# Kernel optimization log

Hardware: AMD Instinct MI355X
Metric: run time of the kernel (lower is better)

## Reference

```python
import jax, jax.numpy as jnp
import numpy as np

SEQ_LEN = 2048
EMB_DIM = 1024
HIDDEN = 1024
VOCAB = 50257
OUT = 50257


def setup_inputs() -> dict:
    key = jax.random.key(0)
    ks = jax.random.split(key, 8)
    s = 0.02
    input_seq = jax.random.randint(ks[0], (SEQ_LEN,), 0, VOCAB)
    emb = jax.random.normal(ks[1], (VOCAB, EMB_DIM), dtype=jnp.float32) * s
    # PyTorch nn.LSTM params: weight_ih [4H, E], weight_hh [4H, H], biases [4H]
    W_ih = jax.random.normal(ks[2], (4 * HIDDEN, EMB_DIM), dtype=jnp.float32) * s
    W_hh = jax.random.normal(ks[3], (4 * HIDDEN, HIDDEN), dtype=jnp.float32) * s
    b_ih = jax.random.normal(ks[4], (4 * HIDDEN,), dtype=jnp.float32) * s
    b_hh = jax.random.normal(ks[5], (4 * HIDDEN,), dtype=jnp.float32) * s
    W_out = jax.random.normal(ks[6], (OUT, HIDDEN), dtype=jnp.float32) * s
    b_out = jax.random.normal(ks[7], (OUT,), dtype=jnp.float32) * s
    return {"input_seq": input_seq, "emb": emb, "W_ih": W_ih, "W_hh": W_hh,
            "b_ih": b_ih, "b_hh": b_hh, "W_out": W_out, "b_out": b_out}


def _lstm_forward(x, W_ih, W_hh, b_ih, b_hh):
    # x: [S, E]; batch dim (=1 in the torch module) is collapsed away.
    H = W_hh.shape[1]
    # Precompute input contribution to all gates for every timestep: [S, 4H]
    x_gates = x @ W_ih.T + (b_ih + b_hh)

    def step(carry, xg):
        h, c = carry
        g = xg + h @ W_hh.T  # [4H]
        i, f, gg, o = jnp.split(g, 4)  # PyTorch gate order: i, f, g, o
        i = jax.nn.sigmoid(i)
        f = jax.nn.sigmoid(f)
        gg = jnp.tanh(gg)
        o = jax.nn.sigmoid(o)
        c = f * c + i * gg
        h = o * jnp.tanh(c)
        return (h, c), h

    h0 = jnp.zeros((H,), dtype=x.dtype)
    c0 = jnp.zeros((H,), dtype=x.dtype)
    _, hs = jax.lax.scan(step, (h0, c0), x_gates)
    return hs  # [S, H]


def reference(input_seq, emb, W_ih, W_hh, b_ih, b_hh, W_out, b_out):
    x = emb[input_seq]  # [S, E] embedding lookup
    hs = _lstm_forward(x, W_ih, W_hh, b_ih, b_hh)  # [S, H]
    logits = hs @ W_out.T + b_out  # [S, OUT]
    return jax.nn.log_softmax(logits, axis=1)
```

## Files before the change

kernel.cpp:

```cpp
#include <hip/hip_runtime.h>
#include <hip/hip_bf16.h>

#define SEQ 2048
#define EMB 1024
#define HID 1024
#define G4  4096
#define VOC 50257
#define VPAD 50304
#define KDIM 1024

typedef short bhalf8 __attribute__((ext_vector_type(8)));
typedef float f32x4  __attribute__((ext_vector_type(4)));

typedef __attribute__((address_space(3))) void lds_void;
typedef __attribute__((address_space(1))) const void gbl_cvoid;

__device__ __forceinline__ void direct_lds16(void* lds, const void* g) {
    __builtin_amdgcn_global_load_lds((gbl_cvoid*)g, (lds_void*)lds, 16, 0, 0);
}

__device__ __forceinline__ unsigned short f2b(float f) {
    unsigned u = __float_as_uint(f);
    unsigned r = u + 0x7fffu + ((u >> 16) & 1u);
    return (unsigned short)(r >> 16);
}

__global__ void f32_to_bf16_k(const float* __restrict__ src, unsigned short* __restrict__ dst,
                              long n_src, long n_dst) {
    long i = ((long)blockIdx.x * 256 + threadIdx.x) * 4;
    if (i >= n_dst) return;
    unsigned short o0 = 0, o1 = 0, o2 = 0, o3 = 0;
    if (i < n_src) {
        f32x4 v = *(const f32x4*)&src[i];
        o0 = f2b(v[0]); o1 = f2b(v[1]); o2 = f2b(v[2]); o3 = f2b(v[3]);
    }
    ushort4 o; o.x = o0; o.y = o1; o.z = o2; o.w = o3;
    *(ushort4*)&dst[i] = o;
}

__global__ void embed_cvt_k(const int* __restrict__ seq, const float* __restrict__ emb,
                            unsigned short* __restrict__ xb) {
    int s = blockIdx.x;
    int k = threadIdx.x * 4;
    long row = (long)seq[s] * EMB;
    f32x4 v = *(const f32x4*)&emb[row + k];
    ushort4 o; o.x = f2b(v[0]); o.y = f2b(v[1]); o.z = f2b(v[2]); o.w = f2b(v[3]);
    *(ushort4*)&xb[(long)s * EMB + k] = o;
}

__global__ void bias_sum_k(const float* __restrict__ a, const float* __restrict__ b,
                           float* __restrict__ o) {
    int i = blockIdx.x * 256 + threadIdx.x;
    if (i < G4) o[i] = a[i] + b[i];
}

__global__ __launch_bounds__(256)
void gemm_bt_k(const unsigned short* __restrict__ A, const unsigned short* __restrict__ Bt,
               const float* __restrict__ bias, float* __restrict__ C,
               int M, int Nreal, int K, int ldc) {
    __shared__ unsigned short lA[128 * 64];
    __shared__ unsigned short lB[128 * 64];
    const int tid  = threadIdx.x;
    const int wave = tid >> 6;
    const int lane = tid & 63;
    const int m0 = blockIdx.x * 128;
    const int n0 = blockIdx.y * 128;
    const int wm = (wave >> 1) * 64;
    const int wn = (wave & 1) * 64;
    const int quad = lane >> 4, l16 = lane & 15;
    const int srow = lane >> 3;
    const int scol = (lane & 7) * 8;

    f32x4 acc[4][4] = {};

    for (int k0 = 0; k0 < K; k0 += 64) {
#pragma unroll
        for (int c = 0; c < 4; ++c) {
            int r0 = wave * 32 + c * 8;
            const unsigned short* ga = A  + (long)(m0 + r0 + srow) * K + k0 + scol;
            direct_lds16(&lA[r0 * 64], ga);
            const unsigned short* gb = Bt + (long)(n0 + r0 + srow) * K + k0 + scol;
            direct_lds16(&lB[r0 * 64], gb);
        }
        __syncthreads();
#pragma unroll
        for (int kk = 0; kk < 2; ++kk) {
            bhalf8 af[4], bf[4];
#pragma unroll
            for (int i = 0; i < 4; ++i) {
                af[i] = *(const bhalf8*)&lA[(wm + i * 16 + l16) * 64 + kk * 32 + quad * 8];
                bf[i] = *(const bhalf8*)&lB[(wn + i * 16 + l16) * 64 + kk * 32 + quad * 8];
            }
#pragma unroll
            for (int i = 0; i < 4; ++i)
#pragma unroll
                for (int j = 0; j < 4; ++j)
                    acc[i][j] = __builtin_amdgcn_mfma_f32_16x16x32_bf16(af[i], bf[j], acc[i][j], 0, 0, 0);
        }
        __syncthreads();
    }
#pragma unroll
    for (int i = 0; i < 4; ++i) {
        int gm = m0 + wm + i * 16 + quad * 4;
#pragma unroll
        for (int j = 0; j < 4; ++j) {
            int gn = n0 + wn + j * 16 + l16;
            if (gn < Nreal) {
                float bv = bias[gn];
#pragma unroll
                for (int r = 0; r < 4; ++r)
                    C[(long)(gm + r) * ldc + gn] = acc[i][j][r] + bv;
            }
        }
    }
}

__global__ __launch_bounds__(256, 1)
void lstm_seq_k(const float* __restrict__ W_hh, const float* __restrict__ xg,
                unsigned short* __restrict__ hs_b, unsigned long long* __restrict__ hbuf) {
    const int tid = threadIdx.x;
    const int wg  = blockIdx.x;
    const int lr  = tid >> 4;
    const int seg = tid & 15;
    const int gate = lr >> 2;
    const int ul   = lr & 3;
    const int u    = wg * 4 + ul;
    const int grow = gate * HID + u;

    __shared__ float h_lds[HID];
    __shared__ float g_lds[4][4];

    f32x4 w[16];
#pragma unroll
    for (int m = 0; m < 16; ++m)
        w[m] = *(const f32x4*)&W_hh[(long)grow * HID + (m * 16 + seg) * 4];

#pragma unroll
    for (int q = 0; q < 4; ++q) h_lds[tid + q * 256] = 0.f;
    float c = 0.f;
    __syncthreads();

    for (int t = 0; t < SEQ; ++t) {
        float xgv = (seg == 0) ? xg[(long)t * G4 + grow] : 0.f;
        if (t > 0) {
            const unsigned long long want = (unsigned long long)t;
            unsigned long long* src = &hbuf[((t - 1) & 1) * HID];
#pragma unroll
            for (int q = 0; q < 4; ++q) {
                int e = tid + q * 256;
                unsigned long long v;
                do {
                    v = __hip_atomic_load(&src[e], __ATOMIC_RELAXED, __HIP_MEMORY_SCOPE_AGENT);
                } while ((v >> 32) != want);
                h_lds[e] = __uint_as_float((unsigned)v);
            }
        }
        __syncthreads();

        float acc = 0.f;
        const f32x4* h4 = (const f32x4*)h_lds;
#pragma unroll
        for (int m = 0; m < 16; ++m) {
            f32x4 hv = h4[m * 16 + seg];
            acc += w[m][0] * hv[0] + w[m][1] * hv[1] + w[m][2] * hv[2] + w[m][3] * hv[3];
        }
        acc += __shfl_xor(acc, 8);
        acc += __shfl_xor(acc, 4);
        acc += __shfl_xor(acc, 2);
        acc += __shfl_xor(acc, 1);

        if (seg == 0) {
            float g = acc + xgv;
            float a = (gate == 2) ? tanhf(g) : 1.f / (1.f + __expf(-g));
            g_lds[gate][ul] = a;
        }
        __syncthreads();
        if (tid < 4) {
            float iv = g_lds[0][tid], fv = g_lds[1][tid], gv = g_lds[2][tid], ov = g_lds[3][tid];
            c = fv * c + iv * gv;
            float h = ov * tanhf(c);
            int ug = wg * 4 + tid;
            hs_b[(long)t * HID + ug] = f2b(h);
            unsigned long long pk = ((unsigned long long)(t + 1) << 32) | (unsigned long long)__float_as_uint(h);
            __hip_atomic_store(&hbuf[(t & 1) * HID + ug], pk, __ATOMIC_RELAXED, __HIP_MEMORY_SCOPE_AGENT);
        }
        __syncthreads();
    }
}

__global__ __launch_bounds__(256)
void log_softmax_k(float* __restrict__ X) {
    const int tid = threadIdx.x;
    const long base = (long)blockIdx.x * VOC;
    float* p = X + base;
    const int head = (4 - (int)(base & 3)) & 3;
    const int n4 = (VOC - head) >> 2;
    const int tail_start = head + n4 * 4;
    f32x4* p4 = (f32x4*)(p + head);

    float m = -INFINITY, s = 0.f;
    auto upd = [&](float x) {
        float nm = fmaxf(m, x);
        s = s * __expf(m - nm) + __expf(x - nm);
        m = nm;
    };
    for (int i = tid; i < n4; i += 256) {
        f32x4 v = p4[i];
        upd(v[0]); upd(v[1]); upd(v[2]); upd(v[3]);
    }
    if (tid == 0) {
        for (int i = 0; i < head; ++i) upd(p[i]);
        for (int i = tail_start; i < VOC; ++i) upd(p[i]);
    }
#pragma unroll
    for (int o = 32; o; o >>= 1) {
        float m2 = __shfl_xor(m, o), s2 = __shfl_xor(s, o);
        float nm = fmaxf(m, m2);
        s = s * __expf(m - nm) + s2 * __expf(m2 - nm);
        m = nm;
    }
    __shared__ float sm[4], ss[4], sL;
    if ((tid & 63) == 0) { sm[tid >> 6] = m; ss[tid >> 6] = s; }
    __syncthreads();
    if (tid == 0) {
        m = sm[0]; s = ss[0];
        for (int wv = 1; wv < 4; ++wv) {
            float m2 = sm[wv], s2 = ss[wv];
            float nm = fmaxf(m, m2);
            s = s * __expf(m - nm) + s2 * __expf(m2 - nm);
            m = nm;
        }
        sL = m + __logf(s);
    }
    __syncthreads();
    const float L = sL;
    for (int i = tid; i < n4; i += 256) {
        f32x4 v = p4[i];
        v[0] -= L; v[1] -= L; v[2] -= L; v[3] -= L;
        p4[i] = v;
    }
    if (tid == 0) {
        for (int i = 0; i < head; ++i) p[i] -= L;
        for (int i = tail_start; i < VOC; ++i) p[i] -= L;
    }
}

extern "C" void kernel_launch(void* const* d_in, const int* in_sizes, int n_in,
                              void* d_out, int out_size, void* d_ws, size_t ws_size,
                              hipStream_t stream) {
    const int*   seq   = (const int*)d_in[0];
    const float* emb   = (const float*)d_in[1];
    const float* W_ih  = (const float*)d_in[2];
    const float* W_hh  = (const float*)d_in[3];
    const float* b_ih  = (const float*)d_in[4];
    const float* b_hh  = (const float*)d_in[5];
    const float* W_out = (const float*)d_in[6];
    const float* b_out = (const float*)d_in[7];
    float* out = (float*)d_out;

    size_t off = 0;
    auto carve = [&](size_t bytes) {
        void* p = (char*)d_ws + off;
        off += (bytes + 255) & ~(size_t)255;
        return p;
    };
    unsigned short* wWout = (unsigned short*)carve((size_t)VPAD * KDIM * 2);
    unsigned short* wWih  = (unsigned short*)carve((size_t)G4 * KDIM * 2);
    unsigned short* wX    = (unsigned short*)carve((size_t)SEQ * EMB * 2);
    unsigned short* wHs   = (unsigned short*)carve((size_t)SEQ * HID * 2);
    float*          wXg   = (float*)carve((size_t)SEQ * G4 * 4);
    float*          wBsum = (float*)carve((size_t)G4 * 4);
    unsigned long long* wHbuf = (unsigned long long*)carve((size_t)2 * HID * 8);

    f32_to_bf16_k<<<(int)(((size_t)VPAD * KDIM / 4 + 255) / 256), 256, 0, stream>>>(
        W_out, wWout, (long)VOC * KDIM, (long)VPAD * KDIM);
    f32_to_bf16_k<<<(int)(((size_t)G4 * KDIM / 4 + 255) / 256), 256, 0, stream>>>(
        W_ih, wWih, (long)G4 * KDIM, (long)G4 * KDIM);
    embed_cvt_k<<<SEQ, 256, 0, stream>>>(seq, emb, wX);
    bias_sum_k<<<(G4 + 255) / 256, 256, 0, stream>>>(b_ih, b_hh, wBsum);

    gemm_bt_k<<<dim3(SEQ / 128, G4 / 128), 256, 0, stream>>>(
        wX, wWih, wBsum, wXg, SEQ, G4, KDIM, G4);

    lstm_seq_k<<<256, 256, 0, stream>>>(W_hh, wXg, wHs, wHbuf);

    gemm_bt_k<<<dim3(SEQ / 128, VPAD / 128), 256, 0, stream>>>(
        wHs, wWout, b_out, out, SEQ, VOC, KDIM, VOC);

    log_softmax_k<<<SEQ, 256, 0, stream>>>(out);
}
```

Baseline: 6.589 ms.

## Restructure LSTM step to one wave per unit with shuffles and double-buffered LDS

Remaps threads so each wave owns one hidden unit's four gates, which lets gate values be exchanged with wave shuffles instead of LDS. Double-buffering the h vector in LDS removes two of the three per-step block barriers, and the hidden-state store now happens before the bf16 output write. The four global polling loads are issued together before any check, the dot product is split into four independent accumulators, and tanh is computed through a scaled sigmoid with fast exp. This shortens the serial critical path of the recurrence, at some cost in tanh accuracy.

```diff
diff --git a/kernel.cpp b/kernel.cpp
--- a/kernel.cpp
+++ b/kernel.cpp
@@ -118,73 +118,86 @@
 __global__ __launch_bounds__(256, 1)
 void lstm_seq_k(const float* __restrict__ W_hh, const float* __restrict__ xg,
                 unsigned short* __restrict__ hs_b, unsigned long long* __restrict__ hbuf) {
-    const int tid = threadIdx.x;
-    const int wg  = blockIdx.x;
-    const int lr  = tid >> 4;
-    const int seg = tid & 15;
-    const int gate = lr >> 2;
-    const int ul   = lr & 3;
-    const int u    = wg * 4 + ul;
+    const int tid  = threadIdx.x;
+    const int wg   = blockIdx.x;
+    const int wave = tid >> 6;
+    const int lane = tid & 63;
+    const int gate = lane >> 4;
+    const int seg  = lane & 15;
+    const int u    = wg * 4 + wave;
     const int grow = gate * HID + u;
 
-    __shared__ float h_lds[HID];
-    __shared__ float g_lds[4][4];
+    __shared__ __align__(16) float h_lds[2][HID];
 
     f32x4 w[16];
 #pragma unroll
     for (int m = 0; m < 16; ++m)
         w[m] = *(const f32x4*)&W_hh[(long)grow * HID + (m * 16 + seg) * 4];
 
-#pragma unroll
-    for (int q = 0; q < 4; ++q) h_lds[tid + q * 256] = 0.f;
+    const float sc = (gate == 2) ? 2.f : 1.f;
+    const float sb = sc - 1.f;
+
+#pragma unroll
+    for (int q = 0; q < 4; ++q) h_lds[0][tid + q * 256] = 0.f;
     float c = 0.f;
-    __syncthreads();
 
     for (int t = 0; t < SEQ; ++t) {
+        const int cur = t & 1;
         float xgv = (seg == 0) ? xg[(long)t * G4 + grow] : 0.f;
         if (t > 0) {
             const unsigned long long want = (unsigned long long)t;
-            unsigned long long* src = &hbuf[((t - 1) & 1) * HID];
-#pragma unroll
-            for (int q = 0; q < 4; ++q) {
-                int e = tid + q * 256;
-                unsigned long long v;
-                do {
-                    v = __hip_atomic_load(&src[e], __ATOMIC_RELAXED, __HIP_MEMORY_SCOPE_AGENT);
-                } while ((v >> 32) != want);
-                h_lds[e] = __uint_as_float((unsigned)v);
-            }
+            const unsigned long long* src = &hbuf[(1 - cur) * HID];
+            const int e0 = tid, e1 = tid + 256, e2 = tid + 512, e3 = tid + 768;
+            unsigned long long v0, v1, v2, v3;
+            do {
+                v0 = __hip_atomic_load(&src[e0], __ATOMIC_RELAXED, __HIP_MEMORY_SCOPE_AGENT);
+                v1 = __hip_atomic_load(&src[e1], __ATOMIC_RELAXED, __HIP_MEMORY_SCOPE_AGENT);
+                v2 = __hip_atomic_load(&src[e2], __ATOMIC_RELAXED, __HIP_MEMORY_SCOPE_AGENT);
+                v3 = __hip_atomic_load(&src[e3], __ATOMIC_RELAXED, __HIP_MEMORY_SCOPE_AGENT);
+            } while (((v0 >> 32) != want) | ((v1 >> 32) != want) |
+                     ((v2 >> 32) != want) | ((v3 >> 32) != want));
+            h_lds[cur][e0] = __uint_as_float((unsigned)v0);
+            h_lds[cur][e1] = __uint_as_float((unsigned)v1);
+            h_lds[cur][e2] = __uint_as_float((unsigned)v2);
+            h_lds[cur][e3] = __uint_as_float((unsigned)v3);
         }
         __syncthreads();
 
-        float acc = 0.f;
-        const f32x4* h4 = (const f32x4*)h_lds;
+        float a0 = 0.f, a1 = 0.f, a2 = 0.f, a3 = 0.f;
+        const f32x4* h4 = (const f32x4*)&h_lds[cur][0];
 #pragma unroll
         for (int m = 0; m < 16; ++m) {
             f32x4 hv = h4[m * 16 + seg];
-            acc += w[m][0] * hv[0] + w[m][1] * hv[1] + w[m][2] * hv[2] + w[m][3] * hv[3];
-        }
+            a0 += w[m][0] * hv[0];
+            a1 += w[m][1] * hv[1];
+            a2 += w[m][2] * hv[2];
+            a3 += w[m][3] * hv[3];
+        }
+        float acc = (a0 + a1) + (a2 + a3);
         acc += __shfl_xor(acc, 8);
         acc += __shfl_xor(acc, 4);
         acc += __shfl_xor(acc, 2);
         acc += __shfl_xor(acc, 1);
 
+        float a = 0.f;
         if (seg == 0) {
             float g = acc + xgv;
-            float a = (gate == 2) ? tanhf(g) : 1.f / (1.f + __expf(-g));
-            g_lds[gate][ul] = a;
-        }
-        __syncthreads();
-        if (tid < 4) {
-            float iv = g_lds[0][tid], fv = g_lds[1][tid], gv = g_lds[2][tid], ov = g_lds[3][tid];
+            float s = 1.f / (1.f + __expf(-sc * g));
+            a = sc * s - sb;
+        }
+        float iv = __shfl(a, 0);
+        float fv = __shfl(a, 16);
+        float gv = __shfl(a, 32);
+        float ov = __shfl(a, 48);
+        if (lane == 0) {
             c = fv * c + iv * gv;
-            float h = ov * tanhf(c);
-            int ug = wg * 4 + tid;
-            hs_b[(long)t * HID + ug] = f2b(h);
-            unsigned long long pk = ((unsigned long long)(t + 1) << 32) | (unsigned long long)__float_as_uint(h);
-            __hip_atomic_store(&hbuf[(t & 1) * HID + ug], pk, __ATOMIC_RELAXED, __HIP_MEMORY_SCOPE_AGENT);
-        }
-        __syncthreads();
+            float th = 2.f / (1.f + __expf(-2.f * c)) - 1.f;
+            float h = ov * th;
+            unsigned long long pk = ((unsigned long long)(t + 1) << 32)
+                                  | (unsigned long long)__float_as_uint(h);
+            __hip_atomic_store(&hbuf[cur * HID + u], pk, __ATOMIC_RELAXED, __HIP_MEMORY_SCOPE_AGENT);
+            hs_b[(long)t * HID + u] = f2b(h);
+        }
     }
 }
 
```

After: 7.905 ms. +20.0%, slower.
